# Optimization experiments

Hardware: AMD Instinct MI355X
Metric: run time of the kernel (lower is better)

Reference implementation:

```python
import jax, jax.numpy as jnp
import numpy as np

B, N, M, D, H, DFF = 1, 2048, 2048, 1024, 16, 4096
MASK_VAL = -50000.0
EPS = 1e-5


def _xavier(k, shape):
    lim = np.sqrt(6.0 / (shape[0] + shape[1])).astype(np.float32)
    return jax.random.uniform(k, shape, jnp.float32, -lim, lim)


def setup_inputs() -> dict:
    key = jax.random.key(0)
    ks = jax.random.split(key, 8)
    return {
        "x": jax.random.normal(ks[0], (B, N, D), jnp.float32),
        "context": jax.random.normal(ks[1], (B, M, D), jnp.float32),
        "Wq": _xavier(ks[2], (D, D)), "bq": jnp.zeros((D,), jnp.float32),
        "Wkv": _xavier(ks[3], (D, 2 * D)), "bkv": jnp.zeros((2 * D,), jnp.float32),
        "Wo": _xavier(ks[4], (D, D)), "bo": jnp.zeros((D,), jnp.float32),
        "ln1_g": jnp.ones((D,), jnp.float32), "ln1_b": jnp.zeros((D,), jnp.float32),
        "W1": _xavier(ks[5], (D, DFF)), "bf1": jnp.zeros((DFF,), jnp.float32),
        "W2": _xavier(ks[6], (DFF, D)), "bf2": jnp.zeros((D,), jnp.float32),
        "ln2_g": jnp.ones((D,), jnp.float32), "ln2_b": jnp.zeros((D,), jnp.float32),
    }


def _layernorm(x, g, b):
    mu = x.mean(-1, keepdims=True)
    var = ((x - mu) ** 2).mean(-1, keepdims=True)
    return (x - mu) * jax.lax.rsqrt(var + EPS) * g + b


def reference(x, context, Wq, bq, Wkv, bkv, Wo, bo, ln1_g, ln1_b, W1, bf1, W2, bf2, ln2_g, ln2_b):
    b, n, d = x.shape
    m = context.shape[1]
    h = H
    dh = d // h
    scale = dh ** -0.5
    # q from x only; k,v from [x; context]
    q = (x @ Wq + bq).reshape(b, n, h, dh).transpose(0, 2, 1, 3)          # b h n dh
    kv_in = jnp.concatenate([x, context], axis=1)                          # b (n+m) d
    k, v = jnp.split(kv_in @ Wkv + bkv, 2, axis=-1)
    k = k.reshape(b, n + m, h, dh).transpose(0, 2, 1, 3)                   # b h (n+m) dh
    v = v.reshape(b, n + m, h, dh).transpose(0, 2, 1, 3)
    dots = jnp.einsum('bhid,bhjd->bhij', q * scale, k)                     # b h n (n+m)
    # causal mask applies only to the self-attention (first n) key columns
    rows = jnp.arange(n)[:, None]
    cols = jnp.arange(n + m)[None, :]
    causal = (cols < n) & (cols > rows)
    dots = jnp.where(causal, MASK_VAL, dots)
    attn = jax.nn.softmax(dots, axis=-1)                                   # dropout = identity (eval)
    out = jnp.einsum('bhij,bhjd->bhid', attn, v)
    out = out.transpose(0, 2, 1, 3).reshape(b, n, d) @ Wo + bo
    # PostNorm(Residual(attn))
    x1 = _layernorm(x + out, ln1_g, ln1_b)
    # PostNorm(Residual(FFN)) with exact-erf GELU
    ff = jax.nn.gelu(x1 @ W1 + bf1, approximate=False) @ W2 + bf2
    return _layernorm(x1 + ff, ln2_g, ln2_b)
```

## Files before the change

### kernel.cpp

```cpp
#include <hip/hip_runtime.h>


using bf16x8 = __attribute__((ext_vector_type(8))) short;
using f32x4  = __attribute__((ext_vector_type(4))) float;

__device__ __forceinline__ ushort f2bf(float f) {
    unsigned u = __float_as_uint(f);
    unsigned r = (u + 0x7fffu + ((u >> 16) & 1u)) >> 16;
    return (ushort)r;
}

__device__ __forceinline__ float bf2f(ushort u) {
    return __uint_as_float((uint)u << 16);
}

__device__ __forceinline__ void gload16(const void* g, void* l) {
    __builtin_amdgcn_global_load_lds(
        (const __attribute__((address_space(1))) void*)g,
        (__attribute__((address_space(3))) void*)l, 16, 0, 0);
}

__device__ __forceinline__ float gelu_erf(float v) {
    return 0.5f * v * (1.0f + erff(v * 0.70710678118654752f));
}

__device__ __forceinline__ uint cvtpk(float a, float b) {
    uint r;
    asm("v_cvt_pk_bf16_f32 %0, %1, %2" : "=v"(r) : "v"(a), "v"(b));
    return r;
}

__global__ __launch_bounds__(256) void cvt_all(const float* __restrict__ in,
                                               ushort* __restrict__ out, int n) {
    for (int i = (blockIdx.x * 256 + threadIdx.x) * 4; i + 3 < n;
         i += gridDim.x * 1024) {
        float4 v = *(const float4*)(in + i);
        ushort4 o;
        o.x = f2bf(v.x); o.y = f2bf(v.y); o.z = f2bf(v.z); o.w = f2bf(v.w);
        *(ushort4*)(out + i) = o;
    }
}

__global__ __launch_bounds__(256) void tcvt_all(
    const float* __restrict__ Wq, const float* __restrict__ Wkv,
    const float* __restrict__ Wo, const float* __restrict__ W1,
    const float* __restrict__ W2,
    ushort* __restrict__ WqT, ushort* __restrict__ WkvT,
    ushort* __restrict__ WoT, ushort* __restrict__ W1T,
    ushort* __restrict__ W2T) {
    __shared__ float tile[32][33];
    int b = blockIdx.x;
    const float* in; ushort* out; int R, C, loc;
    if (b < 1024)      { in = Wq;  out = WqT;  R = 1024; C = 1024; loc = b; }
    else if (b < 3072) { in = Wkv; out = WkvT; R = 1024; C = 2048; loc = b - 1024; }
    else if (b < 4096) { in = Wo;  out = WoT;  R = 1024; C = 1024; loc = b - 3072; }
    else if (b < 8192) { in = W1;  out = W1T;  R = 1024; C = 4096; loc = b - 4096; }
    else               { in = W2;  out = W2T;  R = 4096; C = 1024; loc = b - 8192; }
    const int nbx = C >> 5;
    const int c0 = (loc % nbx) * 32, r0 = (loc / nbx) * 32;
    const int tx = threadIdx.x & 31, ty = threadIdx.x >> 5;
#pragma unroll
    for (int i = 0; i < 4; ++i)
        tile[ty + 8 * i][tx] = in[(size_t)(r0 + ty + 8 * i) * C + c0 + tx];
    __syncthreads();
#pragma unroll
    for (int i = 0; i < 4; ++i)
        out[(size_t)(c0 + ty + 8 * i) * R + r0 + tx] = f2bf(tile[tx][ty + 8 * i]);
}

template <int BM, int BN, int ACT, int OUTF32, int RES, int SCALED, int SPLITK, int VT>
__global__ __launch_bounds__(256) void gemm_bt(
    const ushort* __restrict__ A, int lda, const ushort* __restrict__ Bt, int ldb,
    const float* __restrict__ bias, const float* __restrict__ resid,
    void* __restrict__ Cout, ushort* __restrict__ Vout,
    int M, int N, int K, float scale) {
    constexpr int MR = BM / 32, NR = BN / 32;
    __shared__ __align__(16) ushort Asm[BM * 64];
    __shared__ __align__(16) ushort Bsm[BN * 64];
    const int tid = threadIdx.x;
    const int w = tid >> 6, lane = tid & 63, g = lane >> 4, i15 = lane & 15;
    const int wm = w >> 1, wn = w & 1;
    const int m0 = blockIdx.y * BM, n0 = blockIdx.x * BN;
    if (SPLITK) {
        A += (size_t)blockIdx.z * K;
        Bt += (size_t)blockIdx.z * K;
    }

    f32x4 acc[MR][NR] = {};

    for (int kt = 0; kt < K; kt += 64) {
#pragma unroll
        for (int q = 0; q < BM / 32; ++q) {
            int off = (w * (BM / 32) + q) * 1024 + lane * 16;
            int r = off >> 7, cb = off & 127;
            int scb = cb ^ ((r & 7) << 4);
            const void* src = (const char*)A + ((size_t)(m0 + r) * lda + kt) * 2 + scb;
            gload16(src, (char*)Asm + (w * (BM / 32) + q) * 1024);
        }
#pragma unroll
        for (int q = 0; q < BN / 32; ++q) {
            int off = (w * (BN / 32) + q) * 1024 + lane * 16;
            int r = off >> 7, cb = off & 127;
            int scb = cb ^ ((r & 7) << 4);
            const void* src = (const char*)Bt + ((size_t)(n0 + r) * ldb + kt) * 2 + scb;
            gload16(src, (char*)Bsm + (w * (BN / 32) + q) * 1024);
        }
        __syncthreads();

#pragma unroll
        for (int kc = 0; kc < 2; ++kc) {
            bf16x8 af[MR], bfr[NR];
#pragma unroll
            for (int mi = 0; mi < MR; ++mi) {
                int r = wm * (BM / 2) + mi * 16 + i15;
                af[mi] = *(const bf16x8*)((const char*)Asm + r * 128 +
                                          ((kc * 64 + g * 16) ^ ((r & 7) << 4)));
            }
#pragma unroll
            for (int ni = 0; ni < NR; ++ni) {
                int r = wn * (BN / 2) + ni * 16 + i15;
                bfr[ni] = *(const bf16x8*)((const char*)Bsm + r * 128 +
                                           ((kc * 64 + g * 16) ^ ((r & 7) << 4)));
            }
#pragma unroll
            for (int mi = 0; mi < MR; ++mi)
#pragma unroll
                for (int ni = 0; ni < NR; ++ni)
                    acc[mi][ni] = __builtin_amdgcn_mfma_f32_16x16x32_bf16(
                        af[mi], bfr[ni], acc[mi][ni], 0, 0, 0);
        }
        __syncthreads();
    }

    float* Cf = (float*)Cout;
    if (SPLITK) Cf += (size_t)blockIdx.z * M * N;

#pragma unroll
    for (int ni = 0; ni < NR; ++ni) {
        int col = n0 + wn * (BN / 2) + ni * 16 + i15;
        float bb = bias ? bias[col] : 0.f;
#pragma unroll
        for (int mi = 0; mi < MR; ++mi) {
            if (VT && col >= 1024) {
                int row = m0 + wm * (BM / 2) + mi * 16 + 4 * g;
                ushort4 ov;
                ov.x = f2bf(acc[mi][ni][0] + bb);
                ov.y = f2bf(acc[mi][ni][1] + bb);
                ov.z = f2bf(acc[mi][ni][2] + bb);
                ov.w = f2bf(acc[mi][ni][3] + bb);
                *(ushort4*)(Vout + (size_t)(col - 1024) * 4096 + row) = ov;
            } else {
#pragma unroll
                for (int r2 = 0; r2 < 4; ++r2) {
                    int row = m0 + wm * (BM / 2) + mi * 16 + 4 * g + r2;
                    float v = acc[mi][ni][r2] + bb;
                    if (ACT) v = gelu_erf(v);
                    if (SCALED) v *= scale;
                    size_t off = VT ? ((size_t)row * 1024 + col)
                                    : ((size_t)row * N + col);
                    if (OUTF32) {
                        float rv = RES ? resid[off] : 0.f;
                        Cf[off] = v + rv;
                    } else {
                        ((ushort*)Cout)[off] = f2bf(v);
                    }
                }
            }
        }
    }
}

template <int NS>
__global__ __launch_bounds__(512) void flash_attn(
    const ushort* __restrict__ Q,
    const ushort* __restrict__ Kb,
    const ushort* __restrict__ Vt,
    ushort* __restrict__ O,
    ushort* __restrict__ Opart,
    float* __restrict__ Ml) {
    constexpr int D = 1024;
    __shared__ __align__(16) ushort Ksm[2][64 * 64];
    __shared__ __align__(16) ushort Vsm[2][64 * 64];
    __shared__ __align__(16) ushort Psm[8][16 * 64];

    const int tid = threadIdx.x;
    const int w = tid >> 6, lane = tid & 63, g = lane >> 4, i15 = lane & 15;
    const int bid = blockIdx.x;
    const int h = bid & 15;
    const int qB = 15 - ((bid >> 4) & 15);
    const int s = (NS > 1) ? (bid >> 8) : 0;
    const int qb = qB * 128 + w * 16;
    const int qrow = qb + i15;
    const int diagW = qb >> 6;
    const int diagB = 2 * qB + 1;
    const int nt = diagB + 33;
    const int lo = (s * nt) / NS;
    const int hi = ((s + 1) * nt) / NS;

    bf16x8 qf[2];
    qf[0] = *(const bf16x8*)(Q + (size_t)qrow * D + h * 64 + g * 8);
    qf[1] = *(const bf16x8*)(Q + (size_t)qrow * D + h * 64 + 32 + g * 8);

    f32x4 o[4] = {};
    float m_run = -INFINITY, l_run = 0.f;

    const int sr  = tid >> 3;
    const int scb = (tid & 7) * 16;
    const int ssw = scb ^ ((sr & 7) << 4);
    const char* kb0 = (const char*)Kb + ((size_t)sr * 1024 + h * 64) * 2 + scb;
    const char* vb0 = (const char*)Vt + ((size_t)(h * 64 + sr) * 4096) * 2 + scb;

    uint4 kreg, vreg;
    auto jt_of = [&](int t) { return (t <= diagB) ? t : (32 + (t - diagB - 1)); };
    auto stage = [&](int t) {
        const int jt = jt_of(t);
        kreg = *(const uint4*)(kb0 + (size_t)jt * 64 * 2048);
        vreg = *(const uint4*)(vb0 + (size_t)jt * 128);
    };
    auto wlds = [&](int buf) {
        *(uint4*)((char*)Ksm[buf] + sr * 128 + ssw) = kreg;
        *(uint4*)((char*)Vsm[buf] + sr * 128 + ssw) = vreg;
    };

    const int pbase = i15 * 128;
    const int psw = (i15 & 7) << 4;

    auto body = [&](int buf, int t) {
        const int jt = jt_of(t);
        f32x4 st[4];
        __builtin_amdgcn_s_setprio(1);
#pragma unroll
        for (int jg = 0; jg < 4; ++jg) {
            int jr = jg * 16 + i15;
            bf16x8 ka0 = *(const bf16x8*)((const char*)Ksm[buf] + jr * 128 +
                                          ((g * 16) ^ ((jr & 7) << 4)));
            bf16x8 ka1 = *(const bf16x8*)((const char*)Ksm[buf] + jr * 128 +
                                          ((64 + g * 16) ^ ((jr & 7) << 4)));
            f32x4 z = {};
            z = __builtin_amdgcn_mfma_f32_16x16x32_bf16(ka0, qf[0], z, 0, 0, 0);
            z = __builtin_amdgcn_mfma_f32_16x16x32_bf16(ka1, qf[1], z, 0, 0, 0);
            st[jg] = z;
        }
        __builtin_amdgcn_s_setprio(0);
        if (jt >= diagW && jt <= diagB) {
#pragma unroll
            for (int jg = 0; jg < 4; ++jg)
#pragma unroll
                for (int r = 0; r < 4; ++r) {
                    int j = jt * 64 + jg * 16 + 4 * g + r;
                    if (j > qrow) st[jg][r] = -50000.f;
                }
        }

        float v8[8];
#pragma unroll
        for (int jg = 0; jg < 4; ++jg) {
            v8[2 * jg]     = fmaxf(st[jg][0], st[jg][1]);
            v8[2 * jg + 1] = fmaxf(st[jg][2], st[jg][3]);
        }
        v8[0] = fmaxf(v8[0], v8[4]); v8[1] = fmaxf(v8[1], v8[5]);
        v8[2] = fmaxf(v8[2], v8[6]); v8[3] = fmaxf(v8[3], v8[7]);
        float mt = fmaxf(fmaxf(v8[0], v8[1]), fmaxf(v8[2], v8[3]));
        mt = fmaxf(mt, __shfl_xor(mt, 16));
        mt = fmaxf(mt, __shfl_xor(mt, 32));

        const bool skip = __all(mt - m_run <= 8.f);
        float mnew, fscale;
        if (skip) { mnew = m_run; fscale = 1.f; }
        else      { mnew = fmaxf(m_run, mt); fscale = exp2f(m_run - mnew); }

        float pf[4][4], sj[4];
#pragma unroll
        for (int jg = 0; jg < 4; ++jg) {
#pragma unroll
            for (int r = 0; r < 4; ++r) pf[jg][r] = exp2f(st[jg][r] - mnew);
            sj[jg] = (pf[jg][0] + pf[jg][1]) + (pf[jg][2] + pf[jg][3]);
        }
        float psum = (sj[0] + sj[1]) + (sj[2] + sj[3]);
        psum += __shfl_xor(psum, 16);
        psum += __shfl_xor(psum, 32);
        l_run = l_run * fscale + psum;
        m_run = mnew;

        if (!skip) {
#pragma unroll
            for (int r = 0; r < 4; ++r) {
                float fr = __shfl(fscale, 20 * g + r);
#pragma unroll
                for (int dg = 0; dg < 4; ++dg) o[dg][r] *= fr;
            }
        }

#pragma unroll
        for (int jg = 0; jg < 4; ++jg) {
            uint2 pk;
            pk.x = cvtpk(pf[jg][0], pf[jg][1]);
            pk.y = cvtpk(pf[jg][2], pf[jg][3]);
            *(uint2*)((char*)Psm[w] + pbase + ((jg * 32 + g * 8) ^ psw)) = pk;
        }

        __builtin_amdgcn_s_setprio(1);
#pragma unroll
        for (int jc = 0; jc < 2; ++jc) {
            bf16x8 pa = *(const bf16x8*)((const char*)Psm[w] + pbase +
                                         ((jc * 64 + g * 16) ^ psw));
#pragma unroll
            for (int dg = 0; dg < 4; ++dg) {
                int dr = dg * 16 + i15;
                bf16x8 vb = *(const bf16x8*)((const char*)Vsm[buf] + dr * 128 +
                                             ((jc * 64 + g * 16) ^ ((dr & 7) << 4)));
                o[dg] = __builtin_amdgcn_mfma_f32_16x16x32_bf16(pa, vb, o[dg], 0, 0, 0);
            }
        }
        __builtin_amdgcn_s_setprio(0);
    };

    stage(lo);
    wlds(0);
    __syncthreads();

    int t = lo;
    for (; t + 1 < hi; t += 2) {
        stage(t + 1);
        body(0, t);
        wlds(1);
        __syncthreads();
        if (t + 2 < hi) stage(t + 2);
        body(1, t + 1);
        if (t + 2 < hi) { wlds(0); __syncthreads(); }
    }
    if (t < hi) body(0, t);

    if (NS > 1) {
        if (g == 0) {
            float* mp = Ml + ((size_t)(s * 2048 + qrow) * 16 + h) * 2;
            mp[0] = m_run; mp[1] = l_run;
        }
#pragma unroll
        for (int r = 0; r < 4; ++r)
#pragma unroll
            for (int dg = 0; dg < 4; ++dg) {
                int row = qb + 4 * g + r;
                int col = h * 64 + dg * 16 + i15;
                Opart[(size_t)(s * 2048 + row) * 1024 + col] = f2bf(o[dg][r]);
            }
    } else {
#pragma unroll
        for (int r = 0; r < 4; ++r) {
            float lr = __shfl(l_run, 20 * g + r);
            float inv = 1.f / lr;
#pragma unroll
            for (int dg = 0; dg < 4; ++dg) {
                int row = qb + 4 * g + r;
                int col = h * 64 + dg * 16 + i15;
                O[(size_t)row * D + col] = f2bf(o[dg][r] * inv);
            }
        }
    }
}

template <int NS>
__global__ __launch_bounds__(256) void attn_combine(
    const ushort* __restrict__ Opart, const float* __restrict__ Ml,
    ushort* __restrict__ O) {
    const int row = blockIdx.x, tid = threadIdx.x;
    const int c = tid * 4, h = c >> 6;
    float ms[NS], ls[NS];
#pragma unroll
    for (int s = 0; s < NS; ++s) {
        const float* mp = Ml + ((size_t)(s * 2048 + row) * 16 + h) * 2;
        ms[s] = mp[0]; ls[s] = mp[1];
    }
    float m = ms[0];
#pragma unroll
    for (int s = 1; s < NS; ++s) m = fmaxf(m, ms[s]);
    float denom = 0.f, wgt[NS];
#pragma unroll
    for (int s = 0; s < NS; ++s) { wgt[s] = exp2f(ms[s] - m); denom += ls[s] * wgt[s]; }
    const float inv = 1.f / denom;
    float ax = 0, ay = 0, az = 0, aw = 0;
#pragma unroll
    for (int s = 0; s < NS; ++s) {
        ushort4 a = *(const ushort4*)(Opart + (size_t)(s * 2048 + row) * 1024 + c);
        ax += bf2f(a.x) * wgt[s]; ay += bf2f(a.y) * wgt[s];
        az += bf2f(a.z) * wgt[s]; aw += bf2f(a.w) * wgt[s];
    }
    ushort4 ob;
    ob.x = f2bf(ax * inv); ob.y = f2bf(ay * inv);
    ob.z = f2bf(az * inv); ob.w = f2bf(aw * inv);
    *(ushort4*)(O + (size_t)row * 1024 + c) = ob;
}

__global__ __launch_bounds__(256) void layernorm_k(
    const float* __restrict__ in, const float* __restrict__ gam,
    const float* __restrict__ bet, float* __restrict__ outf,
    ushort* __restrict__ outb) {
    const int row = blockIdx.x, tid = threadIdx.x;
    const float4 v = *(const float4*)(in + (size_t)row * 1024 + tid * 4);
    float s = v.x + v.y + v.z + v.w;
    float sq = v.x * v.x + v.y * v.y + v.z * v.z + v.w * v.w;
#pragma unroll
    for (int d = 1; d < 64; d <<= 1) {
        s += __shfl_xor(s, d);
        sq += __shfl_xor(sq, d);
    }
    __shared__ float red[8];
    const int w = tid >> 6;
    if ((tid & 63) == 0) { red[w] = s; red[4 + w] = sq; }
    __syncthreads();
    s = red[0] + red[1] + red[2] + red[3];
    sq = red[4] + red[5] + red[6] + red[7];
    const float mu = s * (1.f / 1024.f);
    const float rs = rsqrtf(sq * (1.f / 1024.f) - mu * mu + 1e-5f);
    const float4 gg = *(const float4*)(gam + tid * 4);
    const float4 bb = *(const float4*)(bet + tid * 4);
    float4 o;
    o.x = (v.x - mu) * rs * gg.x + bb.x;
    o.y = (v.y - mu) * rs * gg.y + bb.y;
    o.z = (v.z - mu) * rs * gg.z + bb.z;
    o.w = (v.w - mu) * rs * gg.w + bb.w;
    *(float4*)(outf + (size_t)row * 1024 + tid * 4) = o;
    if (outb) {
        ushort4 ob;
        ob.x = f2bf(o.x); ob.y = f2bf(o.y); ob.z = f2bf(o.z); ob.w = f2bf(o.w);
        *(ushort4*)(outb + (size_t)row * 1024 + tid * 4) = ob;
    }
}

template <int NP>
__global__ __launch_bounds__(256) void layernorm_comb(
    const float* __restrict__ P,
    const float* __restrict__ bias, const float* __restrict__ resid,
    const float* __restrict__ gam, const float* __restrict__ bet,
    float* __restrict__ outf) {
    const int row = blockIdx.x, tid = threadIdx.x;
    const float4 rr = *(const float4*)(resid + (size_t)row * 1024 + tid * 4);
    const float4 bs = *(const float4*)(bias + tid * 4);
    float4 v;
    v.x = rr.x + bs.x; v.y = rr.y + bs.y; v.z = rr.z + bs.z; v.w = rr.w + bs.w;
#pragma unroll
    for (int p = 0; p < NP; ++p) {
        const float4 a = *(const float4*)(P + (size_t)(p * 2048 + row) * 1024 + tid * 4);
        v.x += a.x; v.y += a.y; v.z += a.z; v.w += a.w;
    }
    float s = v.x + v.y + v.z + v.w;
    float sq = v.x * v.x + v.y * v.y + v.z * v.z + v.w * v.w;
#pragma unroll
    for (int d = 1; d < 64; d <<= 1) {
        s += __shfl_xor(s, d);
        sq += __shfl_xor(sq, d);
    }
    __shared__ float red[8];
    const int w = tid >> 6;
    if ((tid & 63) == 0) { red[w] = s; red[4 + w] = sq; }
    __syncthreads();
    s = red[0] + red[1] + red[2] + red[3];
    sq = red[4] + red[5] + red[6] + red[7];
    const float mu = s * (1.f / 1024.f);
    const float rs = rsqrtf(sq * (1.f / 1024.f) - mu * mu + 1e-5f);
    const float4 gg = *(const float4*)(gam + tid * 4);
    const float4 bb = *(const float4*)(bet + tid * 4);
    float4 o;
    o.x = (v.x - mu) * rs * gg.x + bb.x;
    o.y = (v.y - mu) * rs * gg.y + bb.y;
    o.z = (v.z - mu) * rs * gg.z + bb.z;
    o.w = (v.w - mu) * rs * gg.w + bb.w;
    *(float4*)(outf + (size_t)row * 1024 + tid * 4) = o;
}

extern "C" void kernel_launch(void* const* d_in, const int* in_sizes, int n_in,
                              void* d_out, int out_size, void* d_ws, size_t ws_size,
                              hipStream_t stream) {
    const float* x    = (const float*)d_in[0];
    const float* ctx  = (const float*)d_in[1];
    const float* Wq   = (const float*)d_in[2];
    const float* bq   = (const float*)d_in[3];
    const float* Wkv  = (const float*)d_in[4];
    const float* bkv  = (const float*)d_in[5];
    const float* Wo   = (const float*)d_in[6];
    const float* bo   = (const float*)d_in[7];
    const float* g1   = (const float*)d_in[8];
    const float* b1   = (const float*)d_in[9];
    const float* W1   = (const float*)d_in[10];
    const float* bf1  = (const float*)d_in[11];
    const float* W2   = (const float*)d_in[12];
    const float* bf2  = (const float*)d_in[13];
    const float* g2   = (const float*)d_in[14];
    const float* b2   = (const float*)d_in[15];

    char* ws = (char*)d_ws;
    const size_t MB = 1u << 20;
    ushort* XCb  = (ushort*)(ws + 0);
    ushort* WoT  = (ushort*)(ws + 8 * MB);
    ushort* W1T  = (ushort*)(ws + 10 * MB);
    ushort* W2T  = (ushort*)(ws + 18 * MB);
    ushort* WqT  = (ushort*)(ws + 26 * MB);
    ushort* WkvT = (ushort*)(ws + 28 * MB);
    ushort* Qs   = (ushort*)(ws + 32 * MB);
    ushort* attn = (ushort*)(ws + 36 * MB);
    ushort* Kb   = (ushort*)(ws + 40 * MB);
    ushort* Vt   = (ushort*)(ws + 48 * MB);
    ushort* x1b  = (ushort*)(ws + 26 * MB);
    float*  x1f  = (float*)(ws + 32 * MB);
    ushort* ffb  = (ushort*)(ws + 40 * MB);
    float*  y1   = (float*)(ws + 56 * MB);
    ushort* Opart = (ushort*)(ws + 64 * MB);
    float*  Pk4   = (float*)(ws + 64 * MB);
    float*  Pk2   = (float*)(ws + 0);

    cvt_all<<<2048, 256, 0, stream>>>(x, XCb, 2048 * 1024);
    cvt_all<<<2048, 256, 0, stream>>>(ctx, XCb + 2048 * 1024, 2048 * 1024);
    tcvt_all<<<12288, 256, 0, stream>>>(Wq, Wkv, Wo, W1, W2,
                                        WqT, WkvT, WoT, W1T, W2T);
    gemm_bt<64, 128, 0, 0, 0, 1, 0, 0><<<dim3(8, 32), 256, 0, stream>>>(
        XCb, 1024, WqT, 1024, bq, nullptr, Qs, nullptr,
        2048, 1024, 1024, 0.18033688011112042f);
    gemm_bt<128, 128, 0, 0, 0, 0, 0, 1><<<dim3(16, 32), 256, 0, stream>>>(
        XCb, 1024, WkvT, 1024, bkv, nullptr, Kb, Vt,
        4096, 2048, 1024, 1.f);

    if (ws_size >= 82 * MB) {
        float* Ml = (float*)(ws + 80 * MB);
        flash_attn<4><<<1024, 512, 0, stream>>>(Qs, Kb, Vt, nullptr, Opart, Ml);
        attn_combine<4><<<2048, 256, 0, stream>>>(Opart, Ml, attn);
    } else if (ws_size >= 73 * MB) {
        float* Ml = (float*)(ws + 72 * MB);
        flash_attn<2><<<512, 512, 0, stream>>>(Qs, Kb, Vt, nullptr, Opart, Ml);
        attn_combine<2><<<2048, 256, 0, stream>>>(Opart, Ml, attn);
    } else {
        flash_attn<1><<<256, 512, 0, stream>>>(Qs, Kb, Vt, attn, nullptr, nullptr);
    }

    gemm_bt<64, 128, 0, 1, 1, 0, 0, 0><<<dim3(8, 32), 256, 0, stream>>>(
        attn, 1024, WoT, 1024, bo, x, y1, nullptr, 2048, 1024, 1024, 1.f);
    layernorm_k<<<2048, 256, 0, stream>>>(y1, g1, b1, x1f, x1b);
    gemm_bt<128, 128, 1, 0, 0, 0, 0, 0><<<dim3(32, 16), 256, 0, stream>>>(
        x1b, 1024, W1T, 1024, bf1, nullptr, ffb, nullptr, 2048, 4096, 1024, 1.f);
    if (ws_size >= 96 * MB) {
        gemm_bt<128, 128, 0, 1, 0, 0, 1, 0><<<dim3(8, 16, 4), 256, 0, stream>>>(
            ffb, 4096, W2T, 4096, nullptr, nullptr, Pk4, nullptr,
            2048, 1024, 1024, 1.f);
        layernorm_comb<4><<<2048, 256, 0, stream>>>(Pk4, bf2, x1f, g2, b2,
                                                    (float*)d_out);
    } else {
        gemm_bt<128, 128, 0, 1, 0, 0, 1, 0><<<dim3(8, 16, 2), 256, 0, stream>>>(
            ffb, 4096, W2T, 4096, nullptr, nullptr, Pk2, nullptr,
            2048, 1024, 2048, 1.f);
        layernorm_comb<2><<<2048, 256, 0, stream>>>(Pk2, bf2, x1f, g2, b2,
                                                    (float*)d_out);
    }
}
```

Measured before the change: 222.7 us.

## Merge prep kernels, MFMA row sums, split-K Wo and bf16 partials

Folds the x/context conversion into the weight-transpose kernel so one launch does all preprocessing. In flash attention, the softmax denominator is now accumulated with an MFMA against a ones vector instead of per-lane sums plus shuffles, and the max tree is reshaped. The Wo projection becomes a 2-way split-K feeding layernorm_comb, which now fuses bias, residual and layernorm and also writes the bf16 copy. The 4-way W2 split-K partials are stored in bf16 instead of f32 to halve that traffic. This costs precision in the FFN partial sums and adds an extra MFMA per P chunk, and the NS=2 attention path is dropped.

```diff
diff --git a/kernel.cpp b/kernel.cpp
--- a/kernel.cpp
+++ b/kernel.cpp
@@ -30,18 +30,9 @@
     return r;
 }
 
-__global__ __launch_bounds__(256) void cvt_all(const float* __restrict__ in,
-                                               ushort* __restrict__ out, int n) {
-    for (int i = (blockIdx.x * 256 + threadIdx.x) * 4; i + 3 < n;
-         i += gridDim.x * 1024) {
-        float4 v = *(const float4*)(in + i);
-        ushort4 o;
-        o.x = f2bf(v.x); o.y = f2bf(v.y); o.z = f2bf(v.z); o.w = f2bf(v.w);
-        *(ushort4*)(out + i) = o;
-    }
-}
-
-__global__ __launch_bounds__(256) void tcvt_all(
+__global__ __launch_bounds__(256) void prep_all(
+    const float* __restrict__ x, const float* __restrict__ ctx,
+    ushort* __restrict__ XCb,
     const float* __restrict__ Wq, const float* __restrict__ Wkv,
     const float* __restrict__ Wo, const float* __restrict__ W1,
     const float* __restrict__ W2,
@@ -50,6 +41,17 @@
     ushort* __restrict__ W2T) {
     __shared__ float tile[32][33];
     int b = blockIdx.x;
+    if (b < 4096) {
+        const float* in = (b < 2048) ? x : ctx;
+        ushort* out = XCb + ((b < 2048) ? 0 : (size_t)2048 * 1024);
+        const int i = ((b & 2047) * 256 + threadIdx.x) * 4;
+        float4 v = *(const float4*)(in + i);
+        ushort4 o;
+        o.x = f2bf(v.x); o.y = f2bf(v.y); o.z = f2bf(v.z); o.w = f2bf(v.w);
+        *(ushort4*)(out + i) = o;
+        return;
+    }
+    b -= 4096;
     const float* in; ushort* out; int R, C, loc;
     if (b < 1024)      { in = Wq;  out = WqT;  R = 1024; C = 1024; loc = b; }
     else if (b < 3072) { in = Wkv; out = WkvT; R = 1024; C = 2048; loc = b - 1024; }
@@ -133,7 +135,11 @@
     }
 
     float* Cf = (float*)Cout;
-    if (SPLITK) Cf += (size_t)blockIdx.z * M * N;
+    ushort* Cb = (ushort*)Cout;
+    if (SPLITK) {
+        Cf += (size_t)blockIdx.z * M * N;
+        Cb += (size_t)blockIdx.z * M * N;
+    }
 
 #pragma unroll
     for (int ni = 0; ni < NR; ++ni) {
@@ -162,7 +168,7 @@
                         float rv = RES ? resid[off] : 0.f;
                         Cf[off] = v + rv;
                     } else {
-                        ((ushort*)Cout)[off] = f2bf(v);
+                        Cb[off] = f2bf(v);
                     }
                 }
             }
@@ -201,8 +207,12 @@
     qf[0] = *(const bf16x8*)(Q + (size_t)qrow * D + h * 64 + g * 8);
     qf[1] = *(const bf16x8*)(Q + (size_t)qrow * D + h * 64 + 32 + g * 8);
 
+    const short oneb = (short)0x3F80;
+    const bf16x8 ones = {oneb, oneb, oneb, oneb, oneb, oneb, oneb, oneb};
+
     f32x4 o[4] = {};
-    float m_run = -INFINITY, l_run = 0.f;
+    f32x4 ls = {};
+    float m_run = -INFINITY;
 
     const int sr  = tid >> 3;
     const int scb = (tid & 7) * 16;
@@ -252,15 +262,14 @@
                 }
         }
 
-        float v8[8];
-#pragma unroll
-        for (int jg = 0; jg < 4; ++jg) {
-            v8[2 * jg]     = fmaxf(st[jg][0], st[jg][1]);
-            v8[2 * jg + 1] = fmaxf(st[jg][2], st[jg][3]);
-        }
-        v8[0] = fmaxf(v8[0], v8[4]); v8[1] = fmaxf(v8[1], v8[5]);
-        v8[2] = fmaxf(v8[2], v8[6]); v8[3] = fmaxf(v8[3], v8[7]);
-        float mt = fmaxf(fmaxf(v8[0], v8[1]), fmaxf(v8[2], v8[3]));
+        float a0 = fmaxf(fmaxf(st[0][0], st[0][1]), st[0][2]);
+        float a1 = fmaxf(fmaxf(st[0][3], st[1][0]), st[1][1]);
+        float a2 = fmaxf(fmaxf(st[1][2], st[1][3]), st[2][0]);
+        float a3 = fmaxf(fmaxf(st[2][1], st[2][2]), st[2][3]);
+        float a4 = fmaxf(fmaxf(st[3][0], st[3][1]), st[3][2]);
+        float b0 = fmaxf(fmaxf(a0, a1), a2);
+        float b1 = fmaxf(fmaxf(a3, a4), st[3][3]);
+        float mt = fmaxf(b0, b1);
         mt = fmaxf(mt, __shfl_xor(mt, 16));
         mt = fmaxf(mt, __shfl_xor(mt, 32));
 
@@ -269,17 +278,11 @@
         if (skip) { mnew = m_run; fscale = 1.f; }
         else      { mnew = fmaxf(m_run, mt); fscale = exp2f(m_run - mnew); }
 
-        float pf[4][4], sj[4];
-#pragma unroll
-        for (int jg = 0; jg < 4; ++jg) {
+        float pf[4][4];
+#pragma unroll
+        for (int jg = 0; jg < 4; ++jg)
 #pragma unroll
             for (int r = 0; r < 4; ++r) pf[jg][r] = exp2f(st[jg][r] - mnew);
-            sj[jg] = (pf[jg][0] + pf[jg][1]) + (pf[jg][2] + pf[jg][3]);
-        }
-        float psum = (sj[0] + sj[1]) + (sj[2] + sj[3]);
-        psum += __shfl_xor(psum, 16);
-        psum += __shfl_xor(psum, 32);
-        l_run = l_run * fscale + psum;
         m_run = mnew;
 
         if (!skip) {
@@ -288,6 +291,7 @@
                 float fr = __shfl(fscale, 20 * g + r);
 #pragma unroll
                 for (int dg = 0; dg < 4; ++dg) o[dg][r] *= fr;
+                ls[r] *= fr;
             }
         }
 
@@ -304,6 +308,7 @@
         for (int jc = 0; jc < 2; ++jc) {
             bf16x8 pa = *(const bf16x8*)((const char*)Psm[w] + pbase +
                                          ((jc * 64 + g * 16) ^ psw));
+            ls = __builtin_amdgcn_mfma_f32_16x16x32_bf16(pa, ones, ls, 0, 0, 0);
 #pragma unroll
             for (int dg = 0; dg < 4; ++dg) {
                 int dr = dg * 16 + i15;
@@ -332,9 +337,12 @@
     if (t < hi) body(0, t);
 
     if (NS > 1) {
-        if (g == 0) {
-            float* mp = Ml + ((size_t)(s * 2048 + qrow) * 16 + h) * 2;
-            mp[0] = m_run; mp[1] = l_run;
+#pragma unroll
+        for (int r = 0; r < 4; ++r) {
+            if (i15 == 4 * g + r) {
+                float* mp = Ml + ((size_t)(s * 2048 + qrow) * 16 + h) * 2;
+                mp[0] = m_run; mp[1] = ls[r];
+            }
         }
 #pragma unroll
         for (int r = 0; r < 4; ++r)
@@ -347,8 +355,7 @@
     } else {
 #pragma unroll
         for (int r = 0; r < 4; ++r) {
-            float lr = __shfl(l_run, 20 * g + r);
-            float inv = 1.f / lr;
+            float inv = 1.f / ls[r];
 #pragma unroll
             for (int dg = 0; dg < 4; ++dg) {
                 int row = qb + 4 * g + r;
@@ -365,18 +372,18 @@
     ushort* __restrict__ O) {
     const int row = blockIdx.x, tid = threadIdx.x;
     const int c = tid * 4, h = c >> 6;
-    float ms[NS], ls[NS];
+    float ms[NS], lsv[NS];
 #pragma unroll
     for (int s = 0; s < NS; ++s) {
         const float* mp = Ml + ((size_t)(s * 2048 + row) * 16 + h) * 2;
-        ms[s] = mp[0]; ls[s] = mp[1];
+        ms[s] = mp[0]; lsv[s] = mp[1];
     }
     float m = ms[0];
 #pragma unroll
     for (int s = 1; s < NS; ++s) m = fmaxf(m, ms[s]);
     float denom = 0.f, wgt[NS];
 #pragma unroll
-    for (int s = 0; s < NS; ++s) { wgt[s] = exp2f(ms[s] - m); denom += ls[s] * wgt[s]; }
+    for (int s = 0; s < NS; ++s) { wgt[s] = exp2f(ms[s] - m); denom += lsv[s] * wgt[s]; }
     const float inv = 1.f / denom;
     float ax = 0, ay = 0, az = 0, aw = 0;
 #pragma unroll
@@ -427,12 +434,12 @@
     }
 }
 
-template <int NP>
+template <int NP, int PBF16, int OUTB>
 __global__ __launch_bounds__(256) void layernorm_comb(
-    const float* __restrict__ P,
+    const void* __restrict__ P,
     const float* __restrict__ bias, const float* __restrict__ resid,
     const float* __restrict__ gam, const float* __restrict__ bet,
-    float* __restrict__ outf) {
+    float* __restrict__ outf, ushort* __restrict__ outb) {
     const int row = blockIdx.x, tid = threadIdx.x;
     const float4 rr = *(const float4*)(resid + (size_t)row * 1024 + tid * 4);
     const float4 bs = *(const float4*)(bias + tid * 4);
@@ -440,8 +447,15 @@
     v.x = rr.x + bs.x; v.y = rr.y + bs.y; v.z = rr.z + bs.z; v.w = rr.w + bs.w;
 #pragma unroll
     for (int p = 0; p < NP; ++p) {
-        const float4 a = *(const float4*)(P + (size_t)(p * 2048 + row) * 1024 + tid * 4);
-        v.x += a.x; v.y += a.y; v.z += a.z; v.w += a.w;
+        if (PBF16) {
+            ushort4 a = *(const ushort4*)((const ushort*)P +
+                          (size_t)(p * 2048 + row) * 1024 + tid * 4);
+            v.x += bf2f(a.x); v.y += bf2f(a.y); v.z += bf2f(a.z); v.w += bf2f(a.w);
+        } else {
+            float4 a = *(const float4*)((const float*)P +
+                          (size_t)(p * 2048 + row) * 1024 + tid * 4);
+            v.x += a.x; v.y += a.y; v.z += a.z; v.w += a.w;
+        }
     }
     float s = v.x + v.y + v.z + v.w;
     float sq = v.x * v.x + v.y * v.y + v.z * v.z + v.w * v.w;
@@ -466,6 +480,11 @@
     o.z = (v.z - mu) * rs * gg.z + bb.z;
     o.w = (v.w - mu) * rs * gg.w + bb.w;
     *(float4*)(outf + (size_t)row * 1024 + tid * 4) = o;
+    if (OUTB) {
+        ushort4 ob;
+        ob.x = f2bf(o.x); ob.y = f2bf(o.y); ob.z = f2bf(o.z); ob.w = f2bf(o.w);
+        *(ushort4*)(outb + (size_t)row * 1024 + tid * 4) = ob;
+    }
 }
 
 extern "C" void kernel_launch(void* const* d_in, const int* in_sizes, int n_in,
@@ -505,12 +524,12 @@
     ushort* ffb  = (ushort*)(ws + 40 * MB);
     float*  y1   = (float*)(ws + 56 * MB);
     ushort* Opart = (ushort*)(ws + 64 * MB);
-    float*  Pk4   = (float*)(ws + 64 * MB);
+    float*  Pwo   = (float*)(ws + 64 * MB);
+    ushort* Pk4b  = (ushort*)(ws + 64 * MB);
     float*  Pk2   = (float*)(ws + 0);
-
-    cvt_all<<<2048, 256, 0, stream>>>(x, XCb, 2048 * 1024);
-    cvt_all<<<2048, 256, 0, stream>>>(ctx, XCb + 2048 * 1024, 2048 * 1024);
-    tcvt_all<<<12288, 256, 0, stream>>>(Wq, Wkv, Wo, W1, W2,
+    float*  Ml    = (float*)(ws + 80 * MB);
+
+    prep_all<<<16384, 256, 0, stream>>>(x, ctx, XCb, Wq, Wkv, Wo, W1, W2,
                                         WqT, WkvT, WoT, W1T, W2T);
     gemm_bt<64, 128, 0, 0, 0, 1, 0, 0><<<dim3(8, 32), 256, 0, stream>>>(
         XCb, 1024, WqT, 1024, bq, nullptr, Qs, nullptr,
@@ -519,34 +538,35 @@
         XCb, 1024, WkvT, 1024, bkv, nullptr, Kb, Vt,
         4096, 2048, 1024, 1.f);
 
-    if (ws_size >= 82 * MB) {
-        float* Ml = (float*)(ws + 80 * MB);
+    const bool big = ws_size >= 82 * MB;
+    if (big) {
         flash_attn<4><<<1024, 512, 0, stream>>>(Qs, Kb, Vt, nullptr, Opart, Ml);
         attn_combine<4><<<2048, 256, 0, stream>>>(Opart, Ml, attn);
-    } else if (ws_size >= 73 * MB) {
-        float* Ml = (float*)(ws + 72 * MB);
-        flash_attn<2><<<512, 512, 0, stream>>>(Qs, Kb, Vt, nullptr, Opart, Ml);
-        attn_combine<2><<<2048, 256, 0, stream>>>(Opart, Ml, attn);
+        gemm_bt<64, 128, 0, 1, 0, 0, 1, 0><<<dim3(8, 32, 2), 256, 0, stream>>>(
+            attn, 1024, WoT, 1024, nullptr, nullptr, Pwo, nullptr,
+            2048, 1024, 512, 1.f);
+        layernorm_comb<2, 0, 1><<<2048, 256, 0, stream>>>(
+            Pwo, bo, x, g1, b1, x1f, x1b);
+        gemm_bt<128, 128, 1, 0, 0, 0, 0, 0><<<dim3(32, 16), 256, 0, stream>>>(
+            x1b, 1024, W1T, 1024, bf1, nullptr, ffb, nullptr,
+            2048, 4096, 1024, 1.f);
+        gemm_bt<128, 128, 0, 0, 0, 0, 1, 0><<<dim3(8, 16, 4), 256, 0, stream>>>(
+            ffb, 4096, W2T, 4096, nullptr, nullptr, Pk4b, nullptr,
+            2048, 1024, 1024, 1.f);
+        layernorm_comb<4, 1, 0><<<2048, 256, 0, stream>>>(
+            Pk4b, bf2, x1f, g2, b2, (float*)d_out, nullptr);
     } else {
         flash_attn<1><<<256, 512, 0, stream>>>(Qs, Kb, Vt, attn, nullptr, nullptr);
-    }
-
-    gemm_bt<64, 128, 0, 1, 1, 0, 0, 0><<<dim3(8, 32), 256, 0, stream>>>(
-        attn, 1024, WoT, 1024, bo, x, y1, nullptr, 2048, 1024, 1024, 1.f);
-    layernorm_k<<<2048, 256, 0, stream>>>(y1, g1, b1, x1f, x1b);
-    gemm_bt<128, 128, 1, 0, 0, 0, 0, 0><<<dim3(32, 16), 256, 0, stream>>>(
-        x1b, 1024, W1T, 1024, bf1, nullptr, ffb, nullptr, 2048, 4096, 1024, 1.f);
-    if (ws_size >= 96 * MB) {
-        gemm_bt<128, 128, 0, 1, 0, 0, 1, 0><<<dim3(8, 16, 4), 256, 0, stream>>>(
-            ffb, 4096, W2T, 4096, nullptr, nullptr, Pk4, nullptr,
-            2048, 1024, 1024, 1.f);
-        layernorm_comb<4><<<2048, 256, 0, stream>>>(Pk4, bf2, x1f, g2, b2,
-                                                    (float*)d_out);
-    } else {
+        gemm_bt<64, 128, 0, 1, 1, 0, 0, 0><<<dim3(8, 32), 256, 0, stream>>>(
+            attn, 1024, WoT, 1024, bo, x, y1, nullptr, 2048, 1024, 1024, 1.f);
+        layernorm_k<<<2048, 256, 0, stream>>>(y1, g1, b1, x1f, x1b);
+        gemm_bt<128, 128, 1, 0, 0, 0, 0, 0><<<dim3(32, 16), 256, 0, stream>>>(
+            x1b, 1024, W1T, 1024, bf1, nullptr, ffb, nullptr,
+            2048, 4096, 1024, 1.f);
         gemm_bt<128, 128, 0, 1, 0, 0, 1, 0><<<dim3(8, 16, 2), 256, 0, stream>>>(
             ffb, 4096, W2T, 4096, nullptr, nullptr, Pk2, nullptr,
             2048, 1024, 2048, 1.f);
-        layernorm_comb<2><<<2048, 256, 0, stream>>>(Pk2, bf2, x1f, g2, b2,
-                                                    (float*)d_out);
-    }
-}
+        layernorm_comb<2, 0, 0><<<2048, 256, 0, stream>>>(
+            Pk2, bf2, x1f, g2, b2, (float*)d_out, nullptr);
+    }
+}
```

Result: faster. 204.4 us (-8.2%).
